# Kernel optimization log

Hardware: AMD Instinct MI355X
Metric: run time of the kernel (lower is better)

Reference implementation:

```python
import jax, jax.numpy as jnp
import numpy as np

NUM_RELS = 8

def _rgcn_layer(x, src, dst, rel, W, Wroot, b, num_rels):
    # PyG RGCNConv with aggr='mean': out = bias + x @ root + sum_r mean_{e in rel r, dst=i} (x[src_e] @ W_r)
    # mean-then-transform == transform-then-mean (linear), so transform first.
    N = x.shape[0]
    xW = jnp.einsum('nf,rfg->rng', x, W)            # [R, N, G] per-relation transformed features
    comb = dst * num_rels + rel                       # combined (node, relation) segment id
    deg = jax.ops.segment_sum(jnp.ones(rel.shape, x.dtype), comb, num_segments=N * num_rels)
    norm = 1.0 / jnp.maximum(deg[comb], 1.0)          # 1/deg_r(dst) per edge
    msg = xW[rel, src] * norm[:, None]                # [E, G]
    agg = jax.ops.segment_sum(msg, dst, num_segments=N)
    return agg + x @ Wroot + b


def setup_inputs() -> dict:
    key = jax.random.key(0)
    ks = jax.random.split(key, 10)
    N, E, R = 50000, 800000, NUM_RELS
    F_in, H, O = 256, 256, 128
    x = jax.random.normal(ks[0], (N, F_in), dtype=jnp.float32)
    edge_index = jax.random.randint(ks[1], (2, E), 0, N, dtype=jnp.int64)
    edge_type = jax.random.randint(ks[2], (E,), 0, R, dtype=jnp.int64)
    s1 = 1.0 / np.sqrt(F_in)
    s2 = 1.0 / np.sqrt(H)
    W1 = jax.random.normal(ks[3], (R, F_in, H), dtype=jnp.float32) * s1
    root1 = jax.random.normal(ks[4], (F_in, H), dtype=jnp.float32) * s1
    b1 = jnp.zeros((H,), dtype=jnp.float32)
    W2 = jax.random.normal(ks[5], (R, H, O), dtype=jnp.float32) * s2
    root2 = jax.random.normal(ks[6], (H, O), dtype=jnp.float32) * s2
    b2 = jnp.zeros((O,), dtype=jnp.float32)
    return {"x": x, "edge_index": edge_index, "edge_type": edge_type,
            "W1": W1, "root1": root1, "b1": b1,
            "W2": W2, "root2": root2, "b2": b2}


def reference(x, edge_index, edge_type, W1, root1, b1, W2, root2, b2):
    src, dst = edge_index[0], edge_index[1]
    h = jax.nn.relu(_rgcn_layer(x, src, dst, edge_type, W1, root1, b1, NUM_RELS))
    return _rgcn_layer(h, src, dst, edge_type, W2, root2, b2, NUM_RELS)
```

## Files before the change

kernel.cpp:

```cpp
#include <hip/hip_runtime.h>
#include <stdint.h>

#define RELS 8
#define F 256
#define KDIM 2304
#define NKT 36
#define TSZ 8192
#define SCAN_CHUNK 1024


typedef __attribute__((ext_vector_type(8))) short short8;
typedef __attribute__((ext_vector_type(4))) float f32x4;
typedef __attribute__((ext_vector_type(2))) unsigned int uint2v;

__device__ __forceinline__ unsigned short f2bf(float f) {
  union { float f; unsigned int u; } v; v.f = f;
  unsigned int u = v.u;
  if ((u & 0x7f800000u) == 0x7f800000u) return (unsigned short)(u >> 16);
  return (unsigned short)((u + 0x7fffu + ((u >> 16) & 1u)) >> 16);
}
__device__ __forceinline__ float bf2f(unsigned short b) {
  union { unsigned int u; float f; } v; v.u = ((unsigned int)b) << 16; return v.f;
}

__global__ void k_xb(const float* __restrict__ x, unsigned short* __restrict__ xb, int N) {
  int tid = blockIdx.x * blockDim.x + threadIdx.x;
  int n = tid >> 6, q = tid & 63;
  if (n >= N) return;
  const float4 v = *(const float4*)&x[(size_t)n * F + q * 4];
  ushort4 o;
  o.x = f2bf(v.x); o.y = f2bf(v.y); o.z = f2bf(v.z); o.w = f2bf(v.w);
  *(ushort4*)&xb[(size_t)n * F + q * 4] = o;
}

__global__ void k_wt(const float* __restrict__ W, const float* __restrict__ root,
                     unsigned short* __restrict__ Wt, int Ncols) {
  int tid = blockIdx.x * blockDim.x + threadIdx.x;
  int total = Ncols * KDIM;
  if (tid >= total) return;
  int n = tid / KDIM, k = tid - n * KDIM;
  float v = (k < 2048) ? W[(size_t)k * Ncols + n] : root[(size_t)(k - 2048) * Ncols + n];
  int tile = n >> 7, row = n & 127;
  int kt = k >> 6, c = k & 63;
  int u = c >> 3, w = c & 7;
  int frag = ((row >> 6) << 3) + (((row >> 4) & 3) << 1) + (u >> 2);
  int dl = ((u & 3) << 4) + (row & 15);
  Wt[(size_t)(tile * NKT + kt) * TSZ + frag * 512 + dl * 8 + w] = f2bf(v);
}

__global__ void k_count(const int* __restrict__ ei, const int* __restrict__ et,
                        int* __restrict__ cnt, int E, int N) {
  int e = blockIdx.x * blockDim.x + threadIdx.x;
  if (e >= E) return;
  int bin = et[e] * N + ei[E + e];
  atomicAdd(&cnt[bin], 1);
}

__global__ void k_scan1(const int* __restrict__ cnt, int* __restrict__ start,
                        int* __restrict__ bsum, int nb) {
  __shared__ int tsum[256];
  const int t = threadIdx.x;
  const int idx = blockIdx.x * SCAN_CHUNK + t * 4;
  int v[4]; int s = 0;
#pragma unroll
  for (int i = 0; i < 4; i++) { v[i] = (idx + i < nb) ? cnt[idx + i] : 0; s += v[i]; }
  tsum[t] = s;
  __syncthreads();
  for (int d = 1; d < 256; d <<= 1) {
    int a = (t >= d) ? tsum[t - d] : 0;
    __syncthreads();
    tsum[t] += a;
    __syncthreads();
  }
  int ex = (t > 0) ? tsum[t - 1] : 0;
#pragma unroll
  for (int i = 0; i < 4; i++) { if (idx + i < nb) start[idx + i] = ex; ex += v[i]; }
  if (t == 255) bsum[blockIdx.x] = tsum[255];
}

__global__ void k_scan2(int* __restrict__ bsum, int nblocks) {
  __shared__ int sh[1024];
  const int t = threadIdx.x;
  sh[t] = (t < nblocks) ? bsum[t] : 0;
  __syncthreads();
  for (int d = 1; d < 1024; d <<= 1) {
    int a = (t >= d) ? sh[t - d] : 0;
    __syncthreads();
    sh[t] += a;
    __syncthreads();
  }
  if (t < nblocks) bsum[t] = (t > 0) ? sh[t - 1] : 0;
  if (t == 1023) bsum[nblocks] = sh[1023];
}

__global__ void k_scan3(int* __restrict__ start, const int* __restrict__ bsum,
                        int nb, int nblocks) {
  int i = blockIdx.x * blockDim.x + threadIdx.x;
  if (i < nb) start[i] += bsum[i >> 10];
  if (i == 0) start[nb] = bsum[nblocks];
}

__global__ void k_scatter(const int* __restrict__ ei, const int* __restrict__ et,
                          const int* __restrict__ start, int* __restrict__ cur,
                          unsigned int* __restrict__ ssrc2, int E, int N) {
  int e = blockIdx.x * blockDim.x + threadIdx.x;
  if (e >= E) return;
  int dst = ei[E + e];
  int bin = et[e] * N + dst;
  int p = atomicAdd(&cur[bin], 1);
  ssrc2[start[bin] + p] = (unsigned)ei[e] | ((unsigned)(dst & 63) << 20);
}

template<int NI, bool RELU, bool OUTBF16>
__global__ __launch_bounds__(256, 2) void k_fused(
    const unsigned short* __restrict__ src, const unsigned short* __restrict__ Wt,
    const int* __restrict__ start, const unsigned int* __restrict__ ssrc2,
    const float* __restrict__ bias, void* __restrict__ outp, int Nn) {
  __shared__ unsigned short slice[4 * 4096];
  const int t = threadIdx.x;
  const int lane = t & 63, wid = t >> 6;
  const int m0 = blockIdx.x * 64;
  const int c15 = lane & 15, quad = lane >> 4;
  const int wn = wid * (NI * 16);
  const int gc = lane >> 4;
  const int gL = lane & 15;
  const int gFragLo = gL >> 3;
  const int gDlHi = ((gL >> 1) & 3) << 4;
  const int gW = (gL & 1) * 4;
  const int gSwz = ((gL >> 1) & 3) << 4;

  f32x4 acc[4][NI];
#pragma unroll
  for (int i = 0; i < 4; i++)
#pragma unroll
    for (int j = 0; j < NI; j++) acc[i][j] = (f32x4)0.f;

  const unsigned short* Bt = Wt + (size_t)(wn >> 7) * NKT * TSZ + lane * 8;
  const int roff = (lane << 3) ^ ((lane >> 4 & 3) << 4);

#define LDPK8(P_, eo_)                                                       \
  { _Pragma("unroll") for (int j = 0; j < 8; j++) {                          \
      int i_ = (eo_) + j; P_[j] = ssrc2[i_ < eEm1 ? i_ : eEm1]; } }
#define LDFV8(Fv_, P_)                                                       \
  { _Pragma("unroll") for (int j = 0; j < 8; j++)                            \
      Fv_[j] = *(const ushort4*)&src[(size_t)(P_[j] & 0xFFFFFu) * F + lane * 4]; }
#define FLUSHROW()                                                           \
  {                                                                          \
    float s_ = 1.0f / (float)(cnt > 1 ? cnt : 1);                            \
    int frag_ = (((curDl >> 4) & 3) << 1) | gFragLo;                         \
    int dloc_ = gDlHi | (curDl & 15);                                        \
    uint2v o_;                                                               \
    o_.x = (unsigned)f2bf(accR.x * s_) | ((unsigned)f2bf(accR.y * s_) << 16);\
    o_.y = (unsigned)f2bf(accR.z * s_) | ((unsigned)f2bf(accR.w * s_) << 16);\
    *(uint2v*)&slice[gc * 4096 + frag_ * 512 + (((dloc_ << 3) | gW) ^ gSwz)] = o_; \
  }
#define PROC(pk_, fv_)                                                       \
  {                                                                          \
    int dl_ = (int)((pk_) >> 20);                                            \
    if (dl_ != curDl) {                                                      \
      if (curDl >= 0) FLUSHROW();                                            \
      curDl = dl_; cnt = 0;                                                  \
      accR.x = 0.f; accR.y = 0.f; accR.z = 0.f; accR.w = 0.f;                \
    }                                                                        \
    accR.x += bf2f((fv_).x); accR.y += bf2f((fv_).y);                        \
    accR.z += bf2f((fv_).z); accR.w += bf2f((fv_).w);                        \
    cnt++;                                                                   \
  }
#define PROC8(P_, Fv_, base_)                                                \
  { _Pragma("unroll") for (int j = 0; j < 8; j++)                            \
      if ((base_) + j < eE) PROC(P_[j], Fv_[j]); }

  for (int r = 0; r < 9; r++) {
    if (r < 8) {
      short8 z8 = {0, 0, 0, 0, 0, 0, 0, 0};
#pragma unroll
      for (int z = 0; z < 8; z++)
        *(short8*)&slice[(z >> 1) * 4096 + (wid * 2 + (z & 1)) * 512 + lane * 8] = z8;

      int rA = m0 + wid * 16;
      int rB = rA + 16;
      rA = rA < Nn ? rA : Nn;
      rB = rB < Nn ? rB : Nn;
      int e = start[r * Nn + rA];
      const int eE = start[r * Nn + rB];

      if (e < eE) {
        const int eEm1 = eE - 1;
        int curDl = -1, cnt = 0;
        f32x4 accR; accR.x = accR.y = accR.z = accR.w = 0.f;

        unsigned pkA[8], pkB[8];
        ushort4 fvA[8], fvB[8];
        LDPK8(pkA, e);     LDFV8(fvA, pkA);
        LDPK8(pkB, e + 8); LDFV8(fvB, pkB);
#pragma unroll 1
        for (int eo = e; eo < eE; eo += 16) {
          PROC8(pkA, fvA, eo);
          LDPK8(pkA, eo + 16); LDFV8(fvA, pkA);
          PROC8(pkB, fvB, eo + 8);
          LDPK8(pkB, eo + 24); LDFV8(fvB, pkB);
        }
        if (curDl >= 0) FLUSHROW();
      }
    } else {
#pragma unroll 4
      for (int bi = 0; bi < 16; bi++) {
        int row = (wid << 4) + bi;
        const uint2v vv = *(const uint2v*)&src[(size_t)(m0 + row) * F + lane * 4];
        int frag = (((row >> 4) & 3) << 1) | gFragLo;
        int dl = gDlHi | (row & 15);
        *(uint2v*)&slice[gc * 4096 + frag * 512 + (((dl << 3) | gW) ^ gSwz)] = vv;
      }
    }
    __syncthreads();
#pragma unroll
    for (int c = 0; c < 4; c++) {
      const unsigned short* bc = Bt + (size_t)(r * 4 + c) * TSZ;
#pragma unroll
      for (int kk = 0; kk < 2; kk++) {
        short8 bfr[NI], afr[4];
#pragma unroll
        for (int ni = 0; ni < NI; ni++) {
          int rB2 = (wn & 127) + ni * 16;
          int fB = ((rB2 >> 6) << 3) + (((rB2 >> 4) & 3) << 1) + kk;
          bfr[ni] = *(const short8*)(bc + fB * 512);
        }
#pragma unroll
        for (int mi = 0; mi < 4; mi++) {
          int fA = (mi << 1) + kk;
          afr[mi] = *(const short8*)&slice[c * 4096 + fA * 512 + roff];
        }
#pragma unroll
        for (int mi = 0; mi < 4; mi++)
#pragma unroll
          for (int ni = 0; ni < NI; ni++)
            acc[mi][ni] = __builtin_amdgcn_mfma_f32_16x16x32_bf16(
                afr[mi], bfr[ni], acc[mi][ni], 0, 0, 0);
      }
    }
    __syncthreads();
  }
#undef LDPK8
#undef LDFV8
#undef FLUSHROW
#undef PROC
#undef PROC8

  const int Nld = NI * 64;
#pragma unroll
  for (int mi = 0; mi < 4; mi++) {
#pragma unroll
    for (int ni = 0; ni < NI; ni++) {
      int n = wn + ni * 16 + c15;
      float bv = bias[n];
#pragma unroll
      for (int rr = 0; rr < 4; rr++) {
        int m = m0 + mi * 16 + quad * 4 + rr;
        if (m < Nn) {
          float v = acc[mi][ni][rr] + bv;
          if (RELU) v = v > 0.f ? v : 0.f;
          if (OUTBF16) ((unsigned short*)outp)[(size_t)m * Nld + n] = f2bf(v);
          else         ((float*)outp)[(size_t)m * Nld + n] = v;
        }
      }
    }
  }
}

extern "C" void kernel_launch(void* const* d_in, const int* in_sizes, int n_in,
                              void* d_out, int out_size, void* d_ws, size_t ws_size,
                              hipStream_t stream) {
  const float* x     = (const float*)d_in[0];
  const int*   ei    = (const int*)d_in[1];
  const int*   et    = (const int*)d_in[2];
  const float* W1    = (const float*)d_in[3];
  const float* root1 = (const float*)d_in[4];
  const float* b1    = (const float*)d_in[5];
  const float* W2    = (const float*)d_in[6];
  const float* root2 = (const float*)d_in[7];
  const float* b2    = (const float*)d_in[8];

  const int N = in_sizes[0] / F;
  const int E = in_sizes[2];
  const int nbins = N * RELS;
  const int Mpad = ((N + 63) / 64) * 64;
  const int nsb = (nbins + SCAN_CHUNK - 1) / SCAN_CHUNK;

  char* base = (char*)d_ws;
  size_t off = 0;
  auto alloc = [&](size_t bytes) {
    void* r = base + off;
    off = (off + bytes + 511) & ~(size_t)511;
    return r;
  };
  unsigned short* Wt1  = (unsigned short*)alloc((size_t)2 * NKT * TSZ * 2);
  unsigned short* Wt2  = (unsigned short*)alloc((size_t)1 * NKT * TSZ * 2);
  int*            cnt  = (int*)alloc((size_t)nbins * 4);
  int*            strt = (int*)alloc((size_t)(nbins + 1) * 4);
  int*            bsum = (int*)alloc((size_t)(nsb + 1) * 4);
  unsigned int*   ssr2 = (unsigned int*)alloc((size_t)E * 4);
  unsigned short* xb   = (unsigned short*)alloc((size_t)Mpad * F * 2);
  unsigned short* h    = (unsigned short*)alloc((size_t)Mpad * F * 2);
  (void)ws_size; (void)n_in; (void)out_size;

  hipMemsetAsync(cnt, 0, (size_t)nbins * 4, stream);
  k_xb<<<(N * 64 + 255) / 256, 256, 0, stream>>>(x, xb, N);
  k_wt<<<(256 * KDIM + 255) / 256, 256, 0, stream>>>(W1, root1, Wt1, 256);
  k_wt<<<(128 * KDIM + 255) / 256, 256, 0, stream>>>(W2, root2, Wt2, 128);
  k_count<<<(E + 255) / 256, 256, 0, stream>>>(ei, et, cnt, E, N);
  k_scan1<<<nsb, 256, 0, stream>>>(cnt, strt, bsum, nbins);
  k_scan2<<<1, 1024, 0, stream>>>(bsum, nsb);
  k_scan3<<<(nbins + 255) / 256, 256, 0, stream>>>(strt, bsum, nbins, nsb);
  hipMemsetAsync(cnt, 0, (size_t)nbins * 4, stream);
  k_scatter<<<(E + 255) / 256, 256, 0, stream>>>(ei, et, strt, cnt, ssr2, E, N);

  k_fused<4, true, true><<<Mpad / 64, 256, 0, stream>>>(xb, Wt1, strt, ssr2, b1, h, N);
  k_fused<2, false, false><<<Mpad / 64, 256, 0, stream>>>(h, Wt2, strt, ssr2, b2, d_out, N);
}
```

Baseline: 546.0 us.

## Use 8 waves per fused block, prefetch next relation's edge packets, merge memsets

The fused gather+GEMM kernel now runs 512 threads (8 waves) per 64-row block. Each wave gathers 8 destination rows instead of 16 and owns half as many output columns (NI halved). The packed edge indices for the next relation are loaded right after the barrier so they overlap the MFMA phase, and the slice zeroing is rewritten per row. On the host, the two counter memsets become one, using a separate cursor array. This trades more waves and more parallel gather latency hiding against higher register and LDS pressure per CU, with launch_bounds(512,2) possibly limiting registers.

```diff
diff --git a/kernel.cpp b/kernel.cpp
--- a/kernel.cpp
+++ b/kernel.cpp
@@ -112,7 +112,7 @@
 }
 
 template<int NI, bool RELU, bool OUTBF16>
-__global__ __launch_bounds__(256, 2) void k_fused(
+__global__ __launch_bounds__(512, 2) void k_fused(
     const unsigned short* __restrict__ src, const unsigned short* __restrict__ Wt,
     const int* __restrict__ start, const unsigned int* __restrict__ ssrc2,
     const float* __restrict__ bias, void* __restrict__ outp, int Nn) {
@@ -169,30 +169,38 @@
 #define PROC8(P_, Fv_, base_)                                                \
   { _Pragma("unroll") for (int j = 0; j < 8; j++)                            \
       if ((base_) + j < eE) PROC(P_[j], Fv_[j]); }
+#define BOUNDS(r_)                                                           \
+  {                                                                          \
+    int rA_ = m0 + wid * 8;                                                  \
+    int rB_ = rA_ + 8;                                                       \
+    rA_ = rA_ < Nn ? rA_ : Nn;                                               \
+    rB_ = rB_ < Nn ? rB_ : Nn;                                               \
+    e = start[(r_) * Nn + rA_];                                              \
+    eE = start[(r_) * Nn + rB_];                                             \
+    eEm1 = (eE > e) ? eE - 1 : 0;                                            \
+  }
+
+  int e, eE, eEm1;
+  unsigned pkA[8], pkB[8];
+  BOUNDS(0);
+  LDPK8(pkA, e); LDPK8(pkB, e + 8);
 
   for (int r = 0; r < 9; r++) {
     if (r < 8) {
-      short8 z8 = {0, 0, 0, 0, 0, 0, 0, 0};
-#pragma unroll
-      for (int z = 0; z < 8; z++)
-        *(short8*)&slice[(z >> 1) * 4096 + (wid * 2 + (z & 1)) * 512 + lane * 8] = z8;
-
-      int rA = m0 + wid * 16;
-      int rB = rA + 16;
-      rA = rA < Nn ? rA : Nn;
-      rB = rB < Nn ? rB : Nn;
-      int e = start[r * Nn + rA];
-      const int eE = start[r * Nn + rB];
-
+#pragma unroll
+      for (int bi = 0; bi < 8; bi++) {
+        int row = wid * 8 + bi;
+        int frag = (((row >> 4) & 3) << 1) | gFragLo;
+        int dl = gDlHi | (row & 15);
+        uint2v z2; z2.x = 0u; z2.y = 0u;
+        *(uint2v*)&slice[gc * 4096 + frag * 512 + (((dl << 3) | gW) ^ gSwz)] = z2;
+      }
       if (e < eE) {
-        const int eEm1 = eE - 1;
         int curDl = -1, cnt = 0;
         f32x4 accR; accR.x = accR.y = accR.z = accR.w = 0.f;
-
-        unsigned pkA[8], pkB[8];
         ushort4 fvA[8], fvB[8];
-        LDPK8(pkA, e);     LDFV8(fvA, pkA);
-        LDPK8(pkB, e + 8); LDFV8(fvB, pkB);
+        LDFV8(fvA, pkA);
+        LDFV8(fvB, pkB);
 #pragma unroll 1
         for (int eo = e; eo < eE; eo += 16) {
           PROC8(pkA, fvA, eo);
@@ -203,9 +211,9 @@
         if (curDl >= 0) FLUSHROW();
       }
     } else {
-#pragma unroll 4
-      for (int bi = 0; bi < 16; bi++) {
-        int row = (wid << 4) + bi;
+#pragma unroll
+      for (int bi = 0; bi < 8; bi++) {
+        int row = wid * 8 + bi;
         const uint2v vv = *(const uint2v*)&src[(size_t)(m0 + row) * F + lane * 4];
         int frag = (((row >> 4) & 3) << 1) | gFragLo;
         int dl = gDlHi | (row & 15);
@@ -213,6 +221,10 @@
       }
     }
     __syncthreads();
+    if (r + 1 < 8) {
+      BOUNDS(r + 1);
+      LDPK8(pkA, e); LDPK8(pkB, e + 8);
+    }
 #pragma unroll
     for (int c = 0; c < 4; c++) {
       const unsigned short* bc = Bt + (size_t)(r * 4 + c) * TSZ;
@@ -245,8 +257,9 @@
 #undef FLUSHROW
 #undef PROC
 #undef PROC8
-
-  const int Nld = NI * 64;
+#undef BOUNDS
+
+  const int Nld = NI * 128;
 #pragma unroll
   for (int mi = 0; mi < 4; mi++) {
 #pragma unroll
@@ -295,15 +308,16 @@
   };
   unsigned short* Wt1  = (unsigned short*)alloc((size_t)2 * NKT * TSZ * 2);
   unsigned short* Wt2  = (unsigned short*)alloc((size_t)1 * NKT * TSZ * 2);
-  int*            cnt  = (int*)alloc((size_t)nbins * 4);
+  int*            cnt  = (int*)alloc((size_t)2 * nbins * 4);
   int*            strt = (int*)alloc((size_t)(nbins + 1) * 4);
   int*            bsum = (int*)alloc((size_t)(nsb + 1) * 4);
   unsigned int*   ssr2 = (unsigned int*)alloc((size_t)E * 4);
   unsigned short* xb   = (unsigned short*)alloc((size_t)Mpad * F * 2);
   unsigned short* h    = (unsigned short*)alloc((size_t)Mpad * F * 2);
+  int* cur = cnt + nbins;
   (void)ws_size; (void)n_in; (void)out_size;
 
-  hipMemsetAsync(cnt, 0, (size_t)nbins * 4, stream);
+  hipMemsetAsync(cnt, 0, (size_t)2 * nbins * 4, stream);
   k_xb<<<(N * 64 + 255) / 256, 256, 0, stream>>>(x, xb, N);
   k_wt<<<(256 * KDIM + 255) / 256, 256, 0, stream>>>(W1, root1, Wt1, 256);
   k_wt<<<(128 * KDIM + 255) / 256, 256, 0, stream>>>(W2, root2, Wt2, 128);
@@ -311,9 +325,8 @@
   k_scan1<<<nsb, 256, 0, stream>>>(cnt, strt, bsum, nbins);
   k_scan2<<<1, 1024, 0, stream>>>(bsum, nsb);
   k_scan3<<<(nbins + 255) / 256, 256, 0, stream>>>(strt, bsum, nbins, nsb);
-  hipMemsetAsync(cnt, 0, (size_t)nbins * 4, stream);
-  k_scatter<<<(E + 255) / 256, 256, 0, stream>>>(ei, et, strt, cnt, ssr2, E, N);
-
-  k_fused<4, true, true><<<Mpad / 64, 256, 0, stream>>>(xb, Wt1, strt, ssr2, b1, h, N);
-  k_fused<2, false, false><<<Mpad / 64, 256, 0, stream>>>(h, Wt2, strt, ssr2, b2, d_out, N);
-}
+  k_scatter<<<(E + 255) / 256, 256, 0, stream>>>(ei, et, strt, cur, ssr2, E, N);
+
+  k_fused<2, true, true><<<Mpad / 64, 512, 0, stream>>>(xb, Wt1, strt, ssr2, b1, h, N);
+  k_fused<1, false, false><<<Mpad / 64, 512, 0, stream>>>(h, Wt2, strt, ssr2, b2, d_out, N);
+}
```

New measurement: 711.5 us. +30.3%, slower.

## Split fused RGCN kernel K-loop across two blocks and combine partials

Applied to the files above, without the earlier changes.

The fused aggregate-plus-GEMM kernel now runs as a 2D grid in which each block handles half of the relation/root K iterations (relations 0-3, or relations 4-7 plus root). Each half writes fp32 partial sums to its own buffer, and a new elementwise kernel adds the two partials plus bias, applying ReLU and bf16 conversion where needed. The aim is to double the block count for better occupancy and latency hiding across the GPU. The cost is two extra launches and a write and read of fp32 partial buffers. The two count memsets are also merged into one.

```diff
diff --git a/kernel.cpp b/kernel.cpp
--- a/kernel.cpp
+++ b/kernel.cpp
@@ -111,15 +111,19 @@
   ssrc2[start[bin] + p] = (unsigned)ei[e] | ((unsigned)(dst & 63) << 20);
 }
 
-template<int NI, bool RELU, bool OUTBF16>
+template<int NI>
 __global__ __launch_bounds__(256, 2) void k_fused(
     const unsigned short* __restrict__ src, const unsigned short* __restrict__ Wt,
     const int* __restrict__ start, const unsigned int* __restrict__ ssrc2,
-    const float* __restrict__ bias, void* __restrict__ outp, int Nn) {
+    float* __restrict__ pout0, float* __restrict__ pout1, int Nn) {
   __shared__ unsigned short slice[4 * 4096];
   const int t = threadIdx.x;
   const int lane = t & 63, wid = t >> 6;
   const int m0 = blockIdx.x * 64;
+  const int half = blockIdx.y;
+  const int r0 = half ? 4 : 0;
+  const int rEnd = half ? 9 : 4;
+  float* __restrict__ pout = half ? pout1 : pout0;
   const int c15 = lane & 15, quad = lane >> 4;
   const int wn = wid * (NI * 16);
   const int gc = lane >> 4;
@@ -170,7 +174,7 @@
   { _Pragma("unroll") for (int j = 0; j < 8; j++)                            \
       if ((base_) + j < eE) PROC(P_[j], Fv_[j]); }
 
-  for (int r = 0; r < 9; r++) {
+  for (int r = r0; r < rEnd; r++) {
     if (r < 8) {
       short8 z8 = {0, 0, 0, 0, 0, 0, 0, 0};
 #pragma unroll
@@ -252,18 +256,36 @@
 #pragma unroll
     for (int ni = 0; ni < NI; ni++) {
       int n = wn + ni * 16 + c15;
-      float bv = bias[n];
 #pragma unroll
       for (int rr = 0; rr < 4; rr++) {
         int m = m0 + mi * 16 + quad * 4 + rr;
-        if (m < Nn) {
-          float v = acc[mi][ni][rr] + bv;
-          if (RELU) v = v > 0.f ? v : 0.f;
-          if (OUTBF16) ((unsigned short*)outp)[(size_t)m * Nld + n] = f2bf(v);
-          else         ((float*)outp)[(size_t)m * Nld + n] = v;
-        }
+        if (m < Nn) pout[(size_t)m * Nld + n] = acc[mi][ni][rr];
       }
     }
+  }
+}
+
+template<int C, bool RELU, bool OUTBF16>
+__global__ void k_comb(const float* __restrict__ p0, const float* __restrict__ p1,
+                       const float* __restrict__ bias, void* __restrict__ outp, int N) {
+  int idx = blockIdx.x * blockDim.x + threadIdx.x;
+  if (idx >= N * (C / 4)) return;
+  int c4 = idx & (C / 4 - 1);
+  const float4 a = *(const float4*)&p0[(size_t)idx * 4];
+  const float4 b = *(const float4*)&p1[(size_t)idx * 4];
+  const float4 bv = *(const float4*)&bias[c4 * 4];
+  float vx = a.x + b.x + bv.x, vy = a.y + b.y + bv.y;
+  float vz = a.z + b.z + bv.z, vw = a.w + b.w + bv.w;
+  if (RELU) {
+    vx = vx > 0.f ? vx : 0.f; vy = vy > 0.f ? vy : 0.f;
+    vz = vz > 0.f ? vz : 0.f; vw = vw > 0.f ? vw : 0.f;
+  }
+  if (OUTBF16) {
+    ushort4 o; o.x = f2bf(vx); o.y = f2bf(vy); o.z = f2bf(vz); o.w = f2bf(vw);
+    *(ushort4*)&((unsigned short*)outp)[(size_t)idx * 4] = o;
+  } else {
+    float4 v; v.x = vx; v.y = vy; v.z = vz; v.w = vw;
+    *(float4*)&((float*)outp)[(size_t)idx * 4] = v;
   }
 }
 
@@ -295,15 +317,18 @@
   };
   unsigned short* Wt1  = (unsigned short*)alloc((size_t)2 * NKT * TSZ * 2);
   unsigned short* Wt2  = (unsigned short*)alloc((size_t)1 * NKT * TSZ * 2);
-  int*            cnt  = (int*)alloc((size_t)nbins * 4);
+  int*            cnt  = (int*)alloc((size_t)2 * nbins * 4);
   int*            strt = (int*)alloc((size_t)(nbins + 1) * 4);
   int*            bsum = (int*)alloc((size_t)(nsb + 1) * 4);
   unsigned int*   ssr2 = (unsigned int*)alloc((size_t)E * 4);
   unsigned short* xb   = (unsigned short*)alloc((size_t)Mpad * F * 2);
   unsigned short* h    = (unsigned short*)alloc((size_t)Mpad * F * 2);
+  float*          p0   = (float*)alloc((size_t)Mpad * 256 * 4);
+  float*          p1   = (float*)alloc((size_t)Mpad * 256 * 4);
+  int* cur = cnt + nbins;
   (void)ws_size; (void)n_in; (void)out_size;
 
-  hipMemsetAsync(cnt, 0, (size_t)nbins * 4, stream);
+  hipMemsetAsync(cnt, 0, (size_t)2 * nbins * 4, stream);
   k_xb<<<(N * 64 + 255) / 256, 256, 0, stream>>>(x, xb, N);
   k_wt<<<(256 * KDIM + 255) / 256, 256, 0, stream>>>(W1, root1, Wt1, 256);
   k_wt<<<(128 * KDIM + 255) / 256, 256, 0, stream>>>(W2, root2, Wt2, 128);
@@ -311,9 +336,10 @@
   k_scan1<<<nsb, 256, 0, stream>>>(cnt, strt, bsum, nbins);
   k_scan2<<<1, 1024, 0, stream>>>(bsum, nsb);
   k_scan3<<<(nbins + 255) / 256, 256, 0, stream>>>(strt, bsum, nbins, nsb);
-  hipMemsetAsync(cnt, 0, (size_t)nbins * 4, stream);
-  k_scatter<<<(E + 255) / 256, 256, 0, stream>>>(ei, et, strt, cnt, ssr2, E, N);
-
-  k_fused<4, true, true><<<Mpad / 64, 256, 0, stream>>>(xb, Wt1, strt, ssr2, b1, h, N);
-  k_fused<2, false, false><<<Mpad / 64, 256, 0, stream>>>(h, Wt2, strt, ssr2, b2, d_out, N);
-}
+  k_scatter<<<(E + 255) / 256, 256, 0, stream>>>(ei, et, strt, cur, ssr2, E, N);
+
+  k_fused<4><<<dim3(Mpad / 64, 2), 256, 0, stream>>>(xb, Wt1, strt, ssr2, p0, p1, N);
+  k_comb<256, true, true><<<(N * 64 + 255) / 256, 256, 0, stream>>>(p0, p1, b1, h, N);
+  k_fused<2><<<dim3(Mpad / 64, 2), 256, 0, stream>>>(h, Wt2, strt, ssr2, p0, p1, N);
+  k_comb<128, false, false><<<(N * 32 + 255) / 256, 256, 0, stream>>>(p0, p1, b2, d_out, N);
+}
```

Result: faster. 506.2 us (-7.3%).
